# Optimization experiments

Measured on AMD Instinct MI355X. Metric: run time of the kernel, lower is better.

## Reference

```python
import jax, jax.numpy as jnp
import numpy as np

B, DIM, CAP, K = 1024, 128, 131072, 16


def setup_inputs() -> dict:
    key = jax.random.key(0)
    k1, k2 = jax.random.split(key)
    x = jax.random.normal(k1, (B, DIM), dtype=jnp.float32)
    memory = jax.random.normal(k2, (CAP, DIM), dtype=jnp.float32)
    return {"x": x, "memory": memory, "k": K}


def reference(x, memory, k):
    # sim: [B, CAP] similarity matrix (dominant memory traffic)
    sim = jnp.matmul(x, memory.T)
    _, idx = jax.lax.top_k(sim, k)          # idx: [B, k]
    # gather k neighbor rows and mean-reduce: [B, k, DIM] -> [B, DIM]
    retrieved = jnp.mean(memory[idx], axis=1)
    return retrieved
```

## Files before the change

### kernel.cpp

```cpp
#include <hip/hip_runtime.h>
#include <hip/hip_bf16.h>
#include <stdint.h>

typedef __attribute__((ext_vector_type(4))) float  float4v;
typedef __attribute__((ext_vector_type(4))) float  f32x4;
typedef __attribute__((ext_vector_type(4))) int    int4v;
typedef __attribute__((ext_vector_type(8))) int    int8v;
typedef __attribute__((ext_vector_type(2))) int    int2v;

#define B_ROWS 1024
#define DIM 128
#define CAP 131072
#define KSEL 16

#define XT 64
#define MT 2048
#define MS 128
#define NCHUNK (CAP / MT)
#define NXT (B_ROWS / XT)
#define ITERS (MT / MS)
#define CAND_BLK 16
#define CAND_CAP 320

#define WS_MEMQ   0u
#define WS_XQ     16777216u
#define WS_THETA  16908288u
#define WS_GCNT   16912384u
#define WS_GCIDX  16916480u

__global__ void k_convert_mem(const float* __restrict__ src, int2v* __restrict__ dst) {
    int t = blockIdx.x * blockDim.x + threadIdx.x;
    const float4v* s4 = ((const float4v*)src) + (size_t)t * 2;
    float4v a = s4[0], b = s4[1];
    int lo = 0, hi = 0;
    lo = __builtin_amdgcn_cvt_pk_fp8_f32(a[0], a[1], lo, false);
    lo = __builtin_amdgcn_cvt_pk_fp8_f32(a[2], a[3], lo, true);
    hi = __builtin_amdgcn_cvt_pk_fp8_f32(b[0], b[1], hi, false);
    hi = __builtin_amdgcn_cvt_pk_fp8_f32(b[2], b[3], hi, true);
    int2v o; o[0] = lo; o[1] = hi;
    dst[t] = o;
}

__global__ void k_prep_x(const float* __restrict__ x, unsigned short* __restrict__ xq,
                         float* __restrict__ theta, int* __restrict__ g_cnt) {
    int row = blockIdx.x, d = threadIdx.x;
    float v = x[(size_t)row * DIM + d];
    float vn = __shfl_down(v, 1);
    if (!(d & 1)) {
        int p = __builtin_amdgcn_cvt_pk_fp8_f32(v, vn, 0, false);
        xq[((size_t)row * DIM + d) >> 1] = (unsigned short)(p & 0xFFFF);
    }
    if (d == 64) g_cnt[row] = 0;
    float s = v * v;
    #pragma unroll
    for (int o = 32; o; o >>= 1) s += __shfl_down(s, o);
    __shared__ float red[2];
    if ((d & 63) == 0) red[d >> 6] = s;
    __syncthreads();
    if (d == 0) theta[row] = 3.2f * sqrtf(red[0] + red[1]);
}

__launch_bounds__(256, 4)
__global__ void k_screen(const unsigned char* __restrict__ memq,
                         const unsigned char* __restrict__ xq,
                         const float* __restrict__ theta,
                         int* __restrict__ g_cnt, int* __restrict__ g_cidx)
{
    __shared__ __align__(1024) unsigned char atile[2][MS * DIM];
    __shared__ __align__(1024) unsigned char xlds[XT * DIM];
    __shared__ int s_cidx[XT * CAND_BLK];
    __shared__ int s_cnt[XT];

    const int t  = threadIdx.x;
    const int l  = t & 63;
    const int w  = t >> 6;
    const int lr = l & 15;
    const int lg = l >> 4;

    const int b     = blockIdx.x;
    const int swz   = (b & 7) * 128 + (b >> 3);
    const int chunk = swz >> 4;
    const int xtile = swz & 15;
    const int xbase = xtile * XT;

    if (t < XT) s_cnt[t] = 0;

    const unsigned char* gsrc0 = memq + (size_t)chunk * MT * DIM;

    #pragma unroll
    for (int i = 0; i < 2; i++) {
        const unsigned char* g = xq + (size_t)xbase * DIM + i * 4096 + w * 1024 + l * 16;
        __builtin_amdgcn_global_load_lds(
            (const __attribute__((address_space(1))) unsigned int*)g,
            (__attribute__((address_space(3))) unsigned int*)(&xlds[0] + i * 4096 + w * 1024), 16, 0, 0);
    }

    auto stage = [&](int it, int buf) {
        const unsigned char* g = gsrc0 + (size_t)it * (MS * DIM);
        #pragma unroll
        for (int i = 0; i < 4; i++) {
            const int slot = i * 4096 + t * 16;
            const int src  = slot ^ (((slot >> 7) & 7) << 4);
            __builtin_amdgcn_global_load_lds(
                (const __attribute__((address_space(1))) unsigned int*)(g + src),
                (__attribute__((address_space(3))) unsigned int*)(&atile[buf][0] + i * 4096 + w * 1024),
                16, 0, 0);
        }
    };

    stage(0, 0);
    __syncthreads();

    int8v bx8[4];
    float th[4];
    #pragma unroll
    for (int ni = 0; ni < 4; ni++) {
        const int xc = ni * 16 + lr;
        th[ni] = theta[xbase + xc];
        int4v blo = *(const int4v*)(&xlds[0] + xc * DIM + lg * 32);
        int4v bhi = *(const int4v*)(&xlds[0] + xc * DIM + lg * 32 + 16);
        bx8[ni] = (int8v){blo[0], blo[1], blo[2], blo[3], bhi[0], bhi[1], bhi[2], bhi[3]};
    }

    for (int it = 0; it < ITERS; it++) {
        __builtin_amdgcn_s_barrier();
        if (it + 1 < ITERS) {
            stage(it + 1, (it + 1) & 1);
            asm volatile("s_waitcnt vmcnt(4)" ::: "memory");
        } else {
            asm volatile("s_waitcnt vmcnt(0)" ::: "memory");
        }
        __builtin_amdgcn_s_barrier();
        __builtin_amdgcn_sched_barrier(0);

        const unsigned char* tb = &atile[it & 1][0];
        #pragma unroll
        for (int mi = 0; mi < 2; mi++) {
            const int r  = mi * 64 + w * 16 + lr;
            const int sw = (r & 7) << 4;
            int4v alo = *(const int4v*)(tb + r * DIM + ((lg * 32) ^ sw));
            int4v ahi = *(const int4v*)(tb + r * DIM + ((lg * 32 + 16) ^ sw));
            int8v a8 = (int8v){alo[0], alo[1], alo[2], alo[3], ahi[0], ahi[1], ahi[2], ahi[3]};

            f32x4 ac[4];
            __builtin_amdgcn_s_setprio(1);
            #pragma unroll
            for (int ni = 0; ni < 4; ni++) {
                ac[ni] = __builtin_amdgcn_mfma_scale_f32_16x16x128_f8f6f4(
                    a8, bx8[ni], (f32x4){0.f, 0.f, 0.f, 0.f},
                    0, 0,
                    0, 0x7F7F7F7Fu,
                    0, 0x7F7F7F7Fu);
            }
            __builtin_amdgcn_s_setprio(0);

            const int mrow0 = chunk * MT + it * MS + mi * 64 + w * 16 + lg * 4;
            #pragma unroll
            for (int ni = 0; ni < 4; ni++) {
                const int c = ni * 16 + lr;
                bool hit = (ac[ni][0] > th[ni]) | (ac[ni][1] > th[ni])
                         | (ac[ni][2] > th[ni]) | (ac[ni][3] > th[ni]);
                if (__builtin_expect(__ballot(hit) != 0ull, 0)) {
                    #pragma unroll
                    for (int j = 0; j < 4; j++) {
                        if (ac[ni][j] > th[ni]) {
                            int slot = atomicAdd(&s_cnt[c], 1);
                            if (slot < CAND_BLK) s_cidx[c * CAND_BLK + slot] = mrow0 + j;
                        }
                    }
                }
            }
        }
    }
    __syncthreads();

    if (t < XT) {
        const int n = min(s_cnt[t], CAND_BLK);
        if (n > 0) {
            const int gcol = xbase + t;
            int base = atomicAdd(&g_cnt[gcol], n);
            for (int s = 0; s < n; s++) {
                int p = base + s;
                if (p < CAND_CAP) g_cidx[gcol * CAND_CAP + p] = s_cidx[t * CAND_BLK + s];
            }
        }
    }
}

__launch_bounds__(512)
__global__ void k_finalize(const float* __restrict__ x, const float* __restrict__ mem,
                           const int* __restrict__ g_cnt, const int* __restrict__ g_cidx,
                           float* __restrict__ out)
{
    const int col = blockIdx.x;
    const int t   = threadIdx.x;
    const int g   = t >> 4;
    const int sl  = t & 15;
    __shared__ double sval[CAND_CAP];
    __shared__ int    sidx[CAND_CAP];
    __shared__ int    ssel[KSEL];

    const int cnt = min(g_cnt[col], CAND_CAP);

    for (int s = t; s < cnt; s += 512) sidx[s] = g_cidx[col * CAND_CAP + s];

    const float* xp = x + (size_t)col * DIM + sl * 8;
    float4v xa = *(const float4v*)xp;
    float4v xc = *(const float4v*)(xp + 4);
    __syncthreads();

    for (int s = g; s < cnt; s += 32) {
        const float* mrow = mem + (size_t)sidx[s] * DIM + sl * 8;
        float4v m0 = *(const float4v*)mrow;
        float4v m1 = *(const float4v*)(mrow + 4);
        double acc = (double)m0[0] * (double)xa[0] + (double)m0[1] * (double)xa[1]
                   + (double)m0[2] * (double)xa[2] + (double)m0[3] * (double)xa[3]
                   + (double)m1[0] * (double)xc[0] + (double)m1[1] * (double)xc[1]
                   + (double)m1[2] * (double)xc[2] + (double)m1[3] * (double)xc[3];
        #pragma unroll
        for (int o = 1; o < 16; o <<= 1) acc += __shfl_xor(acc, o);
        if (sl == 0) sval[s] = acc;
    }
    __syncthreads();

    if (t < 64) {
        for (int r = 0; r < KSEL; r++) {
            double bv = -1.0e301; int bi = 0x7fffffff; int bp = -1;
            for (int s = t; s < cnt; s += 64) {
                double v = sval[s]; int i2 = sidx[s];
                if (v > bv || (v == bv && i2 < bi)) { bv = v; bi = i2; bp = s; }
            }
            #pragma unroll
            for (int o = 32; o; o >>= 1) {
                double ov = __shfl_down(bv, o);
                int    oi = __shfl_down(bi, o);
                int    op = __shfl_down(bp, o);
                if (ov > bv || (ov == bv && oi < bi)) { bv = ov; bi = oi; bp = op; }
            }
            bv = __shfl(bv, 0); bi = __shfl(bi, 0); bp = __shfl(bp, 0);
            if (t == 0) {
                ssel[r] = (bi == 0x7fffffff) ? 0 : bi;
                if (bp >= 0) sval[bp] = -1.0e300;
            }
        }
    }
    __syncthreads();

    if (t < DIM) {
        double a = 0.0;
        #pragma unroll
        for (int r = 0; r < KSEL; r++)
            a += (double)mem[(size_t)ssel[r] * DIM + t];
        out[(size_t)col * DIM + t] = (float)(a * 0.0625);
    }
}

extern "C" void kernel_launch(void* const* d_in, const int* in_sizes, int n_in,
                              void* d_out, int out_size, void* d_ws, size_t ws_size,
                              hipStream_t stream)
{
    const float* x   = (const float*)d_in[0];
    const float* mem = (const float*)d_in[1];
    float* out = (float*)d_out;
    char* ws = (char*)d_ws;

    unsigned char* mem_q = (unsigned char*)(ws + WS_MEMQ);
    unsigned char* x_q   = (unsigned char*)(ws + WS_XQ);
    float* theta = (float*)(ws + WS_THETA);
    int*   g_cnt = (int*)(ws + WS_GCNT);
    int*   g_cidx = (int*)(ws + WS_GCIDX);

    k_prep_x<<<B_ROWS, DIM, 0, stream>>>(x, (unsigned short*)x_q, theta, g_cnt);
    k_convert_mem<<<(CAP * DIM) / (256 * 8), 256, 0, stream>>>(mem, (int2v*)mem_q);
    k_screen<<<NXT * NCHUNK, 256, 0, stream>>>(mem_q, x_q, theta, g_cnt, g_cidx);
    k_finalize<<<B_ROWS, 512, 0, stream>>>(x, mem, g_cnt, g_cidx, out);
}
```

Measured before the change: 91.89 us.

## Widen the query tile, shrink the memory stage, and triple-buffer the screen kernel

The screen kernel now handles 128 query rows per block over 1024-row memory chunks, streamed in 64-row stages, instead of 64 query rows over 2048-row chunks. Each fp8 memory tile is then reused by twice as many query columns, which halves how often each memory row is reloaded across blocks, with the grid size unchanged. The LDS ring grows to three buffers with a prefetch distance of two stages, and the wait counts are adjusted to match, to hide more load latency. The hit test now takes the max of four values before comparing, and the occupancy hint in the launch bounds is dropped. Each wave now holds eight B fragments and eight accumulators, which raises register pressure and may lower occupancy.

```diff
diff --git a/kernel.cpp b/kernel.cpp
--- a/kernel.cpp
+++ b/kernel.cpp
@@ -13,11 +13,11 @@
 #define CAP 131072
 #define KSEL 16
 
-#define XT 64
-#define MT 2048
-#define MS 128
+#define XT 128
+#define MT 1024
+#define MS 64
 #define NCHUNK (CAP / MT)
-#define NXT (B_ROWS / XT)
+#define NXTB (B_ROWS / XT)
 #define ITERS (MT / MS)
 #define CAND_BLK 16
 #define CAND_CAP 320
@@ -60,13 +60,13 @@
     if (d == 0) theta[row] = 3.2f * sqrtf(red[0] + red[1]);
 }
 
-__launch_bounds__(256, 4)
+__launch_bounds__(256)
 __global__ void k_screen(const unsigned char* __restrict__ memq,
                          const unsigned char* __restrict__ xq,
                          const float* __restrict__ theta,
                          int* __restrict__ g_cnt, int* __restrict__ g_cidx)
 {
-    __shared__ __align__(1024) unsigned char atile[2][MS * DIM];
+    __shared__ __align__(1024) unsigned char atile[3][MS * DIM];
     __shared__ __align__(1024) unsigned char xlds[XT * DIM];
     __shared__ int s_cidx[XT * CAND_BLK];
     __shared__ int s_cnt[XT];
@@ -79,8 +79,8 @@
 
     const int b     = blockIdx.x;
     const int swz   = (b & 7) * 128 + (b >> 3);
-    const int chunk = swz >> 4;
-    const int xtile = swz & 15;
+    const int chunk = swz >> 3;
+    const int xtile = swz & 7;
     const int xbase = xtile * XT;
 
     if (t < XT) s_cnt[t] = 0;
@@ -88,7 +88,7 @@
     const unsigned char* gsrc0 = memq + (size_t)chunk * MT * DIM;
 
     #pragma unroll
-    for (int i = 0; i < 2; i++) {
+    for (int i = 0; i < 4; i++) {
         const unsigned char* g = xq + (size_t)xbase * DIM + i * 4096 + w * 1024 + l * 16;
         __builtin_amdgcn_global_load_lds(
             (const __attribute__((address_space(1))) unsigned int*)g,
@@ -98,7 +98,7 @@
     auto stage = [&](int it, int buf) {
         const unsigned char* g = gsrc0 + (size_t)it * (MS * DIM);
         #pragma unroll
-        for (int i = 0; i < 4; i++) {
+        for (int i = 0; i < 2; i++) {
             const int slot = i * 4096 + t * 16;
             const int src  = slot ^ (((slot >> 7) & 7) << 4);
             __builtin_amdgcn_global_load_lds(
@@ -109,64 +109,66 @@
     };
 
     stage(0, 0);
-    __syncthreads();
-
-    int8v bx8[4];
-    float th[4];
+    stage(1, 1);
+    asm volatile("s_waitcnt vmcnt(0)" ::: "memory");
+    __syncthreads();
+
+    int8v bx8[8];
+    float th[8];
     #pragma unroll
-    for (int ni = 0; ni < 4; ni++) {
+    for (int ni = 0; ni < 8; ni++) {
         const int xc = ni * 16 + lr;
         th[ni] = theta[xbase + xc];
         int4v blo = *(const int4v*)(&xlds[0] + xc * DIM + lg * 32);
         int4v bhi = *(const int4v*)(&xlds[0] + xc * DIM + lg * 32 + 16);
         bx8[ni] = (int8v){blo[0], blo[1], blo[2], blo[3], bhi[0], bhi[1], bhi[2], bhi[3]};
     }
+    const f32x4 zc = {0.f, 0.f, 0.f, 0.f};
 
     for (int it = 0; it < ITERS; it++) {
+        const int buf = it % 3;
         __builtin_amdgcn_s_barrier();
-        if (it + 1 < ITERS) {
-            stage(it + 1, (it + 1) & 1);
+        if (it + 2 < ITERS) {
+            stage(it + 2, (it + 2) % 3);
             asm volatile("s_waitcnt vmcnt(4)" ::: "memory");
+        } else if (it + 1 < ITERS) {
+            asm volatile("s_waitcnt vmcnt(2)" ::: "memory");
         } else {
             asm volatile("s_waitcnt vmcnt(0)" ::: "memory");
         }
         __builtin_amdgcn_s_barrier();
         __builtin_amdgcn_sched_barrier(0);
 
-        const unsigned char* tb = &atile[it & 1][0];
-        #pragma unroll
-        for (int mi = 0; mi < 2; mi++) {
-            const int r  = mi * 64 + w * 16 + lr;
-            const int sw = (r & 7) << 4;
-            int4v alo = *(const int4v*)(tb + r * DIM + ((lg * 32) ^ sw));
-            int4v ahi = *(const int4v*)(tb + r * DIM + ((lg * 32 + 16) ^ sw));
-            int8v a8 = (int8v){alo[0], alo[1], alo[2], alo[3], ahi[0], ahi[1], ahi[2], ahi[3]};
-
-            f32x4 ac[4];
-            __builtin_amdgcn_s_setprio(1);
-            #pragma unroll
-            for (int ni = 0; ni < 4; ni++) {
-                ac[ni] = __builtin_amdgcn_mfma_scale_f32_16x16x128_f8f6f4(
-                    a8, bx8[ni], (f32x4){0.f, 0.f, 0.f, 0.f},
-                    0, 0,
-                    0, 0x7F7F7F7Fu,
-                    0, 0x7F7F7F7Fu);
-            }
-            __builtin_amdgcn_s_setprio(0);
-
-            const int mrow0 = chunk * MT + it * MS + mi * 64 + w * 16 + lg * 4;
-            #pragma unroll
-            for (int ni = 0; ni < 4; ni++) {
-                const int c = ni * 16 + lr;
-                bool hit = (ac[ni][0] > th[ni]) | (ac[ni][1] > th[ni])
-                         | (ac[ni][2] > th[ni]) | (ac[ni][3] > th[ni]);
-                if (__builtin_expect(__ballot(hit) != 0ull, 0)) {
-                    #pragma unroll
-                    for (int j = 0; j < 4; j++) {
-                        if (ac[ni][j] > th[ni]) {
-                            int slot = atomicAdd(&s_cnt[c], 1);
-                            if (slot < CAND_BLK) s_cidx[c * CAND_BLK + slot] = mrow0 + j;
-                        }
+        const unsigned char* tb = &atile[buf][0];
+        const int r  = w * 16 + lr;
+        const int sw = (r & 7) << 4;
+        int4v alo = *(const int4v*)(tb + r * DIM + ((lg * 32) ^ sw));
+        int4v ahi = *(const int4v*)(tb + r * DIM + ((lg * 32 + 16) ^ sw));
+        int8v a8 = (int8v){alo[0], alo[1], alo[2], alo[3], ahi[0], ahi[1], ahi[2], ahi[3]};
+
+        f32x4 ac[8];
+        __builtin_amdgcn_s_setprio(1);
+        #pragma unroll
+        for (int ni = 0; ni < 8; ni++) {
+            ac[ni] = __builtin_amdgcn_mfma_scale_f32_16x16x128_f8f6f4(
+                a8, bx8[ni], zc,
+                0, 0,
+                0, 0x7F7F7F7Fu,
+                0, 0x7F7F7F7Fu);
+        }
+        __builtin_amdgcn_s_setprio(0);
+
+        const int mrow0 = chunk * MT + it * MS + w * 16 + lg * 4;
+        #pragma unroll
+        for (int ni = 0; ni < 8; ni++) {
+            const int c = ni * 16 + lr;
+            float m = fmaxf(fmaxf(ac[ni][0], ac[ni][1]), fmaxf(ac[ni][2], ac[ni][3]));
+            if (__builtin_expect(__ballot(m > th[ni]) != 0ull, 0)) {
+                #pragma unroll
+                for (int j = 0; j < 4; j++) {
+                    if (ac[ni][j] > th[ni]) {
+                        int slot = atomicAdd(&s_cnt[c], 1);
+                        if (slot < CAND_BLK) s_cidx[c * CAND_BLK + slot] = mrow0 + j;
                     }
                 }
             }
@@ -272,6 +274,6 @@
 
     k_prep_x<<<B_ROWS, DIM, 0, stream>>>(x, (unsigned short*)x_q, theta, g_cnt);
     k_convert_mem<<<(CAP * DIM) / (256 * 8), 256, 0, stream>>>(mem, (int2v*)mem_q);
-    k_screen<<<NXT * NCHUNK, 256, 0, stream>>>(mem_q, x_q, theta, g_cnt, g_cidx);
+    k_screen<<<NXTB * NCHUNK, 256, 0, stream>>>(mem_q, x_q, theta, g_cnt, g_cidx);
     k_finalize<<<B_ROWS, 512, 0, stream>>>(x, mem, g_cnt, g_cidx, out);
 }
```

After: 87.92 us. 1.05x faster.
